# Kernel optimization log

Hardware: AMD Instinct MI355X
Metric: run time of the kernel (lower is better)

The kernel has to match this reference:

```python
import jax, jax.numpy as jnp
import numpy as np

N = 100000
E = 1600000
IN_C = 128
HID = 32
HEADS = 4
OUT_C = 16
G = 128
NEG_SLOPE = 0.2


def setup_inputs() -> dict:
    key = jax.random.key(0)
    ks = jax.random.split(key, 16)
    x = jax.random.normal(ks[0], (N, IN_C), dtype=jnp.float32)
    edge_index = jax.random.randint(ks[1], (2, E), 0, N, dtype=jnp.int64)
    batch = jnp.sort(jax.random.randint(ks[2], (N,), 0, G, dtype=jnp.int64))
    node_weights = jax.random.uniform(ks[3], (N, 1), dtype=jnp.float32)
    s = 1.0 / np.sqrt(IN_C)
    W1 = jax.random.uniform(ks[4], (IN_C, HEADS * HID), jnp.float32, -s, s)
    att_src1 = jax.random.uniform(ks[5], (HEADS, HID), jnp.float32, -s, s)
    att_dst1 = jax.random.uniform(ks[6], (HEADS, HID), jnp.float32, -s, s)
    b1 = jnp.zeros((HEADS * HID,), jnp.float32)
    s2 = 1.0 / np.sqrt(HEADS * HID)
    W2 = jax.random.uniform(ks[7], (HEADS * HID, HID), jnp.float32, -s2, s2)
    att_src2 = jax.random.uniform(ks[8], (1, HID), jnp.float32, -s2, s2)
    att_dst2 = jax.random.uniform(ks[9], (1, HID), jnp.float32, -s2, s2)
    b2 = jnp.zeros((HID,), jnp.float32)
    s3 = 1.0 / np.sqrt(HID)
    fcW = jax.random.uniform(ks[10], (HID, OUT_C), jnp.float32, -s3, s3)
    fcb = jax.random.uniform(ks[11], (OUT_C,), jnp.float32, -s3, s3)
    return {"x": x, "edge_index": edge_index, "batch": batch,
            "node_weights": node_weights,
            "W1": W1, "att_src1": att_src1, "att_dst1": att_dst1, "b1": b1,
            "W2": W2, "att_src2": att_src2, "att_dst2": att_dst2, "b2": b2,
            "fcW": fcW, "fcb": fcb}


def gat_conv(x, src, dst, W, att_src, att_dst, bias, heads, ch, concat):
    n = x.shape[0]
    h = (x @ W).reshape(n, heads, ch)                       # [N,H,C]
    a_src = jnp.sum(h * att_src[None], axis=-1)             # [N,H]
    a_dst = jnp.sum(h * att_dst[None], axis=-1)             # [N,H]
    e = jax.nn.leaky_relu(a_src[src] + a_dst[dst], NEG_SLOPE)  # [E,H]
    # segment softmax over incoming edges of each destination node
    e_max = jax.ops.segment_max(e, dst, num_segments=n)
    ex = jnp.exp(e - e_max[dst])
    denom = jax.ops.segment_sum(ex, dst, num_segments=n)
    alpha = ex / denom[dst]                                 # [E,H]
    msg = h[src] * alpha[..., None]                         # [E,H,C]
    out = jax.ops.segment_sum(msg, dst, num_segments=n)     # [N,H,C]
    if concat:
        out = out.reshape(n, heads * ch)
    else:
        out = out.mean(axis=1)
    return out + bias


def reference(x, edge_index, batch, node_weights,
              W1, att_src1, att_dst1, b1,
              W2, att_src2, att_dst2, b2,
              fcW, fcb):
    n = x.shape[0]
    # PyG GATConv adds self-loops by default
    loop = jnp.arange(n, dtype=edge_index.dtype)
    src = jnp.concatenate([edge_index[0], loop])
    dst = jnp.concatenate([edge_index[1], loop])

    h = x * node_weights
    h = jax.nn.elu(gat_conv(h, src, dst, W1, att_src1, att_dst1, b1, HEADS, HID, True))
    h = jax.nn.elu(gat_conv(h, src, dst, W2, att_src2, att_dst2, b2, 1, HID, False))
    # global mean pool over graphs
    sums = jax.ops.segment_sum(h, batch, num_segments=G)
    cnts = jax.ops.segment_sum(jnp.ones((n,), h.dtype), batch, num_segments=G)
    pooled = sums / jnp.maximum(cnts, 1.0)[:, None]
    return pooled @ fcW + fcb
```

## Files before the change

kernel.cpp:

```cpp
#include <hip/hip_runtime.h>
#include <cstdint>

#define NGRAPH 128
#define NEG 0.2f
#define NB_MAX 512
#define BSH 8
#define BSZ 256
#define CAP 8192
#define CH  2048

typedef unsigned int uint;
typedef unsigned short ushort;
typedef unsigned char uchar;
typedef __attribute__((ext_vector_type(8))) short bf16x8;
typedef __attribute__((ext_vector_type(4))) float f32x4;
typedef __attribute__((ext_vector_type(2))) float f32x2;

union U4B { uint4 u; bf16x8 v; };

__device__ __forceinline__ ushort f2bf(float f) {
  uint u = __float_as_uint(f);
  uint r = (u + 0x7FFF + ((u >> 16) & 1)) >> 16;
  return (ushort)r;
}

__device__ __forceinline__ uint cvtpkbf16(float lo, float hi) {
  uint r;
  asm("v_cvt_pk_bf16_f32 %0, %1, %2" : "=v"(r) : "v"(lo), "v"(hi));
  return r;
}

__device__ __forceinline__ void pkfma(f32x2& acc, f32x2 f, f32x2 w) {
  asm("v_pk_fma_f32 %0, %1, %2, %0" : "+v"(acc) : "v"(f), "v"(w));
}

__device__ __forceinline__ float bperm_f(int addr, float v) {
  return __int_as_float(__builtin_amdgcn_ds_bpermute(addr, __float_as_int(v)));
}
__device__ __forceinline__ int bperm_i(int addr, int v) {
  return __builtin_amdgcn_ds_bpermute(addr, v);
}

__device__ __forceinline__ int wave_incl_scan_i(int v) {
  int lane = threadIdx.x & 63;
#pragma unroll
  for (int off = 1; off < 64; off <<= 1) {
    int u = __shfl_up(v, off, 64);
    if (lane >= off) v += u;
  }
  return v;
}

__global__ void k_bin(const int* __restrict__ ei,
                      const float* __restrict__ W1, const float* __restrict__ W2,
                      ushort* __restrict__ Wt1, ushort* __restrict__ Wt2,
                      int E, int Etot, int NB, int nbin,
                      int* __restrict__ bcur, uint* __restrict__ bbuf) {
  if (blockIdx.x >= (uint)nbin) {
    int t2 = (blockIdx.x - nbin) * 256 + threadIdx.x;
    if (t2 < 16384) {
      int n = t2 >> 7, k = t2 & 127;
      Wt1[t2] = f2bf(W1[k * 128 + n]);
    } else {
      int u = t2 - 16384;
      int n = u >> 7, k = u & 127;
      Wt2[u] = f2bf(W2[k * 32 + n]);
    }
    return;
  }
  __shared__ int h[NB_MAX];
  __shared__ int baseo[NB_MAX];
  __shared__ uint crec[CH];
  __shared__ ushort cbkt[CH];
  int t = threadIdx.x;
  for (int b = t; b < NB; b += 256) h[b] = 0;
  __syncthreads();
  int cbase = blockIdx.x * CH;
  int cend = min(cbase + CH, Etot);
  int nch = cend - cbase;
  for (int i = t; i < nch; i += 256) {
    int e = cbase + i;
    int s, d;
    if (e < E) {
      s = __builtin_nontemporal_load(&ei[e]);
      d = __builtin_nontemporal_load(&ei[E + e]);
    } else { s = e - E; d = s; }
    int b = d >> BSH;
    crec[i] = ((uint)(d & (BSZ - 1)) << 17) | (uint)s;
    cbkt[i] = (ushort)b;
    atomicAdd(&h[b], 1);
  }
  __syncthreads();
  for (int b = t; b < NB; b += 256) {
    int c = h[b];
    baseo[b] = c ? atomicAdd(&bcur[b], c) : 0;
    h[b] = 0;
  }
  __syncthreads();
  for (int i = t; i < nch; i += 256) {
    int b = cbkt[i];
    int r = atomicAdd(&h[b], 1);
    bbuf[(size_t)b * CAP + baseo[b] + r] = crec[i];
  }
}

__global__ void k_bg(const uint* __restrict__ bbuf, const int* __restrict__ bcur,
                     int NB, int N, int* __restrict__ offs, int* __restrict__ ssrc,
                     const float* __restrict__ x, const ushort* __restrict__ Wt,
                     const float* __restrict__ nw, const float* __restrict__ att_s,
                     const float* __restrict__ att_d, uchar* __restrict__ hb1,
                     float* __restrict__ asrc, float* __restrict__ adst) {
  __shared__ int sst[NB_MAX + 1];
  __shared__ int wsum2[4];
  __shared__ int deg[BSZ];
  if (blockIdx.x < (uint)NB) {
    int t = threadIdx.x, lane = t & 63, wid = t >> 6;
    int v0 = (2 * t < NB) ? bcur[2 * t] : 0;
    int v1 = (2 * t + 1 < NB) ? bcur[2 * t + 1] : 0;
    int s = v0 + v1;
    int sv = wave_incl_scan_i(s);
    if (lane == 63) wsum2[wid] = sv;
    deg[t] = 0;
    __syncthreads();
    if (t == 0) {
      int r = 0;
#pragma unroll
      for (int k = 0; k < 4; k++) { int x2 = wsum2[k]; wsum2[k] = r; r += x2; }
    }
    __syncthreads();
    int excl = wsum2[wid] + sv - s;
    sst[2 * t] = excl;
    sst[2 * t + 1] = excl + v0;
    if (t == 255) sst[512] = excl + v0 + v1;
    __syncthreads();
    int b = blockIdx.x;
    int ebeg = sst[b], eend = sst[b + 1];
    int cnt = eend - ebeg;
    const uint* brow = bbuf + (size_t)b * CAP;
    for (int i = t; i < cnt; i += BSZ)
      atomicAdd(&deg[brow[i] >> 17], 1);
    __syncthreads();
    int v = deg[t];
    int sv2 = wave_incl_scan_i(v);
    if (lane == 63) wsum2[wid] = sv2;
    __syncthreads();
    if (t == 0) {
      int r = 0;
#pragma unroll
      for (int k = 0; k < 4; k++) { int x2 = wsum2[k]; wsum2[k] = r; r += x2; }
    }
    __syncthreads();
    int excl2 = wsum2[wid] + sv2 - v;
    int node = (b << BSH) + t;
    if (node < N) offs[node] = ebeg + excl2;
    if (b == 0 && t == 0) offs[N] = sst[512];
    __syncthreads();
    deg[t] = excl2;
    __syncthreads();
    for (int i = t; i < cnt; i += BSZ) {
      uint rec = brow[i];
      int r = atomicAdd(&deg[rec >> 17], 1);
      ssrc[ebeg + r] = (int)(rec & 0x1FFFF);
    }
    return;
  }
  int bid = blockIdx.x - NB;
  int wv = threadIdx.x >> 6, l = threadIdx.x & 63;
  int lg = l >> 4, lr = l & 15;
  int row0 = bid * 64 + wv * 16;
  int node = row0 + lr;
  bool valid = node < N;
  float sc = valid ? nw[node] : 0.f;
  bf16x8 xfr[4];
  const float* xr = x + (size_t)node * 128;
#pragma unroll
  for (int kc = 0; kc < 4; kc++) {
    float v[8];
    if (valid) {
      f32x4 q0 = __builtin_nontemporal_load(reinterpret_cast<const f32x4*>(xr + kc * 32 + lg * 8));
      f32x4 q1 = __builtin_nontemporal_load(reinterpret_cast<const f32x4*>(xr + kc * 32 + lg * 8 + 4));
      v[0] = q0[0]; v[1] = q0[1]; v[2] = q0[2]; v[3] = q0[3];
      v[4] = q1[0]; v[5] = q1[1]; v[6] = q1[2]; v[7] = q1[3];
    } else {
#pragma unroll
      for (int j = 0; j < 8; j++) v[j] = 0.f;
    }
    U4B a;
    a.u.x = cvtpkbf16(v[0] * sc, v[1] * sc);
    a.u.y = cvtpkbf16(v[2] * sc, v[3] * sc);
    a.u.z = cvtpkbf16(v[4] * sc, v[5] * sc);
    a.u.w = cvtpkbf16(v[6] * sc, v[7] * sc);
    xfr[kc] = a.v;
  }
  float pS[4] = {}, pD[4] = {};
#pragma unroll
  for (int ct = 0; ct < 8; ct++) {
    f32x4 acc = {0.f, 0.f, 0.f, 0.f};
    const ushort* wrow = Wt + (size_t)(ct * 16 + lr) * 128;
#pragma unroll
    for (int kc = 0; kc < 4; kc++) {
      U4B bfr;
      bfr.u = *reinterpret_cast<const uint4*>(wrow + kc * 32 + lg * 8);
      acc = __builtin_amdgcn_mfma_f32_16x16x32_bf16(bfr.v, xfr[kc], acc, 0, 0, 0);
    }
    int c0 = ct * 16 + lg * 4;
    if (valid) {
      uint u8 = (uint)__builtin_amdgcn_cvt_pk_fp8_f32(acc[0], acc[1], 0, false);
      u8 = (uint)__builtin_amdgcn_cvt_pk_fp8_f32(acc[2], acc[3], u8, true);
      *reinterpret_cast<uint*>(hb1 + (size_t)node * 128 + c0) = u8;
    }
    float4 as4 = *reinterpret_cast<const float4*>(att_s + c0);
    float4 ad4 = *reinterpret_cast<const float4*>(att_d + c0);
    int h = ct >> 1;
    pS[h] += acc[0] * as4.x + acc[1] * as4.y + acc[2] * as4.z + acc[3] * as4.w;
    pD[h] += acc[0] * ad4.x + acc[1] * ad4.y + acc[2] * ad4.z + acc[3] * ad4.w;
  }
#pragma unroll
  for (int off = 16; off < 64; off <<= 1) {
#pragma unroll
    for (int h = 0; h < 4; h++) {
      pS[h] += __shfl_xor(pS[h], off, 64);
      pD[h] += __shfl_xor(pD[h], off, 64);
    }
  }
  if (lg == 0 && valid) {
    *reinterpret_cast<float4*>(asrc + node * 4) = make_float4(pS[0], pS[1], pS[2], pS[3]);
    *reinterpret_cast<float4*>(adst + node * 4) = make_float4(pD[0], pD[1], pD[2], pD[3]);
  }
}

__global__ void k_aggr1(const int* __restrict__ offs, const int* __restrict__ ssrc,
                        const uchar* __restrict__ hb, const float* __restrict__ asrc,
                        const float* __restrict__ adst, const float* __restrict__ bias,
                        const ushort* __restrict__ Wt2, const float* __restrict__ as2,
                        const float* __restrict__ ad2, uchar* __restrict__ rec2,
                        float* __restrict__ adst2, int N) {
  __shared__ ushort rowl[4][136];
  int tid = threadIdx.x;
  int wv = tid >> 6, l = tid & 63;
  int d = blockIdx.x * 4 + wv;
  int dc = min(d, N - 1);
  int slot = l >> 3;
  int cb = l & 7;
  int h = cb >> 1;
  int hq = l & 3;
  int eidx = l >> 2;
  float adq = adst[dc * 4 + hq];
  int beg = offs[dc], end = offs[dc + 1];
  int endm1 = end - 1;
  const uchar* hbc = hb + cb * 16;
  int bp0 = (slot * 4 + h) << 2;
  int bp1 = bp0 + 128;
  f32x2 a2[8] = {};
  float dsp = 0.f;
  auto ACC = [&](uint4 p, float w) {
    f32x2 wp = {w, w};
    f32x2 f;
    f = __builtin_amdgcn_cvt_pk_f32_fp8(p.x, false); pkfma(a2[0], f, wp);
    f = __builtin_amdgcn_cvt_pk_f32_fp8(p.x, true);  pkfma(a2[1], f, wp);
    f = __builtin_amdgcn_cvt_pk_f32_fp8(p.y, false); pkfma(a2[2], f, wp);
    f = __builtin_amdgcn_cvt_pk_f32_fp8(p.y, true);  pkfma(a2[3], f, wp);
    f = __builtin_amdgcn_cvt_pk_f32_fp8(p.z, false); pkfma(a2[4], f, wp);
    f = __builtin_amdgcn_cvt_pk_f32_fp8(p.z, true);  pkfma(a2[5], f, wp);
    f = __builtin_amdgcn_cvt_pk_f32_fp8(p.w, false); pkfma(a2[6], f, wp);
    f = __builtin_amdgcn_cvt_pk_f32_fp8(p.w, true);  pkfma(a2[7], f, wp);
  };
  for (int base = beg; base < end; base += 32) {
    int eA = base + eidx;
    int eB = eA + 16;
    int sA = ssrc[min(eA, endm1)];
    int sB = ssrc[min(eB, endm1)];
    int s0 = bperm_i(bp0, sA);
    int s1 = bperm_i(bp1, sA);
    int s2 = bperm_i(bp0, sB);
    int s3 = bperm_i(bp1, sB);
    int rem = end - base;
    uint4 p0, p1, p2, p3;
    p0 = *reinterpret_cast<const uint4*>(hbc + (size_t)s0 * 128);
    if (rem > 8)  p1 = *reinterpret_cast<const uint4*>(hbc + (size_t)s1 * 128);
    if (rem > 16) p2 = *reinterpret_cast<const uint4*>(hbc + (size_t)s2 * 128);
    if (rem > 24) p3 = *reinterpret_cast<const uint4*>(hbc + (size_t)s3 * 128);
    float aA = asrc[sA * 4 + hq] + adq;
    float aB = asrc[sB * 4 + hq] + adq;
    aA = fmaxf(aA, aA * NEG);
    aB = fmaxf(aB, aB * NEG);
    float wA = (eA < end) ? __expf(aA) : 0.f;
    float wB = (eB < end) ? __expf(aB) : 0.f;
    dsp += wA + wB;
    float w0 = bperm_f(bp0, wA);
    float w1 = bperm_f(bp1, wA);
    float w2 = bperm_f(bp0, wB);
    float w3 = bperm_f(bp1, wB);
    ACC(p0, w0);
    if (rem > 8)  ACC(p1, w1);
    if (rem > 16) ACC(p2, w2);
    if (rem > 24) ACC(p3, w3);
  }
  dsp += __shfl_xor(dsp, 4, 64);
  dsp += __shfl_xor(dsp, 8, 64);
  dsp += __shfl_xor(dsp, 16, 64);
  dsp += __shfl_xor(dsp, 32, 64);
  float ds = bperm_f(h << 2, dsp);
  int b3 = (l >> 3) & 1, b4 = (l >> 4) & 1, b5 = (l >> 5) & 1;
  float t8[8];
#pragma unroll
  for (int r = 0; r < 8; r++) {
    float av = a2[r >> 1][r & 1];
    float bv = a2[(r + 8) >> 1][r & 1];
    float send = b3 ? av : bv;
    float recv = __shfl_xor(send, 8, 64);
    t8[r] = (b3 ? bv : av) + recv;
  }
  float t4[4];
#pragma unroll
  for (int r = 0; r < 4; r++) {
    float send = b4 ? t8[r] : t8[r + 4];
    float recv = __shfl_xor(send, 16, 64);
    t4[r] = (b4 ? t8[r + 4] : t8[r]) + recv;
  }
  float t2[2];
#pragma unroll
  for (int r = 0; r < 2; r++) {
    float send = b5 ? t4[r] : t4[r + 2];
    float recv = __shfl_xor(send, 32, 64);
    t2[r] = (b5 ? t4[r + 2] : t4[r]) + recv;
  }
  float inv = __builtin_amdgcn_rcpf(ds > 0.f ? ds : 1.f);
  int c0 = cb * 16 + b3 * 8 + b4 * 4 + b5 * 2;
  float2 bi = *reinterpret_cast<const float2*>(bias + c0);
  float r0 = fmaf(t2[0], inv, bi.x);
  float r1 = fmaf(t2[1], inv, bi.y);
  r0 = r0 > 0.f ? r0 : __expf(r0) - 1.f;
  r1 = r1 > 0.f ? r1 : __expf(r1) - 1.f;
  *reinterpret_cast<uint*>(&rowl[wv][c0]) = cvtpkbf16(r0, r1);
  __syncthreads();
  if (wv != 0) return;
  int lg = l >> 4, lr = l & 15;
  int rsel = lr & 3;
  bf16x8 bfrag[4];
#pragma unroll
  for (int kc = 0; kc < 4; kc++) {
    U4B bb;
    bb.u = *reinterpret_cast<const uint4*>(&rowl[rsel][kc * 32 + lg * 8]);
    bfrag[kc] = bb.v;
  }
  int dd = blockIdx.x * 4 + lr;
  bool vs = (lr < 4) && (dd < N);
  float pS = 0.f, pD = 0.f;
#pragma unroll
  for (int ct = 0; ct < 2; ct++) {
    f32x4 acc = {0.f, 0.f, 0.f, 0.f};
    const ushort* wrow = Wt2 + (size_t)(ct * 16 + lr) * 128;
#pragma unroll
    for (int kc = 0; kc < 4; kc++) {
      U4B bfr;
      bfr.u = *reinterpret_cast<const uint4*>(wrow + kc * 32 + lg * 8);
      acc = __builtin_amdgcn_mfma_f32_16x16x32_bf16(bfr.v, bfrag[kc], acc, 0, 0, 0);
    }
    int cg = ct * 16 + lg * 4;
    if (vs) {
      uint u8 = (uint)__builtin_amdgcn_cvt_pk_fp8_f32(acc[0], acc[1], 0, false);
      u8 = (uint)__builtin_amdgcn_cvt_pk_fp8_f32(acc[2], acc[3], u8, true);
      *reinterpret_cast<uint*>(rec2 + (size_t)dd * 64 + cg) = u8;
    }
    float4 as4 = *reinterpret_cast<const float4*>(as2 + cg);
    float4 ad4 = *reinterpret_cast<const float4*>(ad2 + cg);
    pS += acc[0] * as4.x + acc[1] * as4.y + acc[2] * as4.z + acc[3] * as4.w;
    pD += acc[0] * ad4.x + acc[1] * ad4.y + acc[2] * ad4.z + acc[3] * ad4.w;
  }
  pS += __shfl_xor(pS, 16, 64);
  pS += __shfl_xor(pS, 32, 64);
  pD += __shfl_xor(pD, 16, 64);
  pD += __shfl_xor(pD, 32, 64);
  if (vs && lg == 0) {
    *reinterpret_cast<float*>(rec2 + (size_t)dd * 64 + 32) = pS;
    adst2[dd] = pD;
  }
}

__global__ void k_aggr2(const int* __restrict__ offs, const int* __restrict__ ssrc,
                        const uchar* __restrict__ rec, const float* __restrict__ adst,
                        const float* __restrict__ bias, const int* __restrict__ batch,
                        float* __restrict__ gsum, int N) {
  __shared__ float sblk[4][32];
  int tid = threadIdx.x;
  int wid = tid >> 6, l = tid & 63;
  if (tid < 128) sblk[tid >> 5][tid & 31] = 0.f;
  __syncthreads();
  int d = blockIdx.x * 4 + wid;
  bool valid = d < N;
  int dc = valid ? d : N - 1;
  int slot = l >> 2;
  int k = l & 3;
  float ad = adst[dc];
  int beg = offs[dc];
  int end = valid ? offs[dc + 1] : beg;
  int endm1 = end - 1;
  const uchar* rk = rec + k * 8;
  int bq0 = slot << 2;
  int bq1 = (slot + 16) << 2;
  int bq2 = (slot + 32) << 2;
  int bq3 = (slot + 48) << 2;
  f32x2 a2[4] = {};
  float dsp = 0.f;
  auto ACC2 = [&](uint2 p, float w) {
    f32x2 wp = {w, w};
    f32x2 f;
    f = __builtin_amdgcn_cvt_pk_f32_fp8(p.x, false); pkfma(a2[0], f, wp);
    f = __builtin_amdgcn_cvt_pk_f32_fp8(p.x, true);  pkfma(a2[1], f, wp);
    f = __builtin_amdgcn_cvt_pk_f32_fp8(p.y, false); pkfma(a2[2], f, wp);
    f = __builtin_amdgcn_cvt_pk_f32_fp8(p.y, true);  pkfma(a2[3], f, wp);
  };
  for (int base = beg; base < end; base += 64) {
    int e = base + l;
    int sL = ssrc[min(e, endm1)];
    int s0 = bperm_i(bq0, sL);
    int s1 = bperm_i(bq1, sL);
    int s2 = bperm_i(bq2, sL);
    int s3 = bperm_i(bq3, sL);
    int rem = end - base;
    float av = *reinterpret_cast<const float*>(rec + (size_t)sL * 64 + 32);
    uint2 p0, p1, p2, p3;
    p0 = *reinterpret_cast<const uint2*>(rk + (size_t)s0 * 64);
    if (rem > 16) p1 = *reinterpret_cast<const uint2*>(rk + (size_t)s1 * 64);
    if (rem > 32) p2 = *reinterpret_cast<const uint2*>(rk + (size_t)s2 * 64);
    if (rem > 48) p3 = *reinterpret_cast<const uint2*>(rk + (size_t)s3 * 64);
    float xv = av + ad;
    xv = fmaxf(xv, xv * NEG);
    float wL = (e < end) ? __expf(xv) : 0.f;
    dsp += wL;
    float w0 = bperm_f(bq0, wL);
    float w1 = bperm_f(bq1, wL);
    float w2 = bperm_f(bq2, wL);
    float w3 = bperm_f(bq3, wL);
    ACC2(p0, w0);
    if (rem > 16) ACC2(p1, w1);
    if (rem > 32) ACC2(p2, w2);
    if (rem > 48) ACC2(p3, w3);
  }
  dsp += __shfl_xor(dsp, 1, 64);
  dsp += __shfl_xor(dsp, 2, 64);
  dsp += __shfl_xor(dsp, 4, 64);
  dsp += __shfl_xor(dsp, 8, 64);
  dsp += __shfl_xor(dsp, 16, 64);
  dsp += __shfl_xor(dsp, 32, 64);
  int b2 = (l >> 2) & 1, b3 = (l >> 3) & 1, b4 = (l >> 4) & 1;
  float t4[4];
#pragma unroll
  for (int r = 0; r < 4; r++) {
    float av = a2[r >> 1][r & 1];
    float bv = a2[(r + 4) >> 1][r & 1];
    float send = b2 ? av : bv;
    float recv = __shfl_xor(send, 4, 64);
    t4[r] = (b2 ? bv : av) + recv;
  }
  float t2[2];
#pragma unroll
  for (int r = 0; r < 2; r++) {
    float send = b3 ? t4[r] : t4[r + 2];
    float recv = __shfl_xor(send, 8, 64);
    t2[r] = (b3 ? t4[r + 2] : t4[r]) + recv;
  }
  float send = b4 ? t2[0] : t2[1];
  float recv = __shfl_xor(send, 16, 64);
  float t1 = (b4 ? t2[1] : t2[0]) + recv;
  t1 += __shfl_xor(t1, 32, 64);
  int gfirst = batch[blockIdx.x * 4];
  if (l < 32 && valid) {
    int c = k * 8 + b2 * 4 + b3 * 2 + b4;
    float inv = __builtin_amdgcn_rcpf(dsp > 0.f ? dsp : 1.f);
    float r = fmaf(t1, inv, bias[c]);
    r = r > 0.f ? r : __expf(r) - 1.f;
    int g = batch[dc];
    int sl = g - gfirst;
    if (sl < 4) atomicAdd(&sblk[sl][c], r);
    else atomicAdd(&gsum[g * 32 + c], r);
  }
  __syncthreads();
  if (tid < 128) {
    int sl = tid >> 5, c = tid & 31;
    float v = sblk[sl][c];
    int gg = gfirst + sl;
    if (v != 0.f && gg < NGRAPH) atomicAdd(&gsum[gg * 32 + c], v);
  }
}

__global__ void k_fc(const float* __restrict__ gsum, const int* __restrict__ batch,
                     const float* __restrict__ fcW, const float* __restrict__ fcb,
                     float* __restrict__ out, int N) {
  int g = blockIdx.x;
  int l = threadIdx.x;
  int lo = 0, hi = N;
  while (lo < hi) { int mid = (lo + hi) >> 1; if (batch[mid] < g) lo = mid + 1; else hi = mid; }
  int beg = lo;
  hi = N;
  while (lo < hi) { int mid = (lo + hi) >> 1; if (batch[mid] < g + 1) lo = mid + 1; else hi = mid; }
  int end = lo;
  float inv = 1.f / fmaxf((float)(end - beg), 1.f);
  __shared__ float pooled[32];
  if (l < 32) pooled[l] = gsum[g * 32 + l] * inv;
  __syncthreads();
  if (l < 16) {
    float r = fcb[l];
#pragma unroll
    for (int cc = 0; cc < 32; cc++) r += pooled[cc] * fcW[cc * 16 + l];
    out[g * 16 + l] = r;
  }
}

extern "C" void kernel_launch(void* const* d_in, const int* in_sizes, int n_in,
                              void* d_out, int out_size, void* d_ws, size_t ws_size,
                              hipStream_t stream) {
  const float* x     = (const float*)d_in[0];
  const int*   ei    = (const int*)d_in[1];
  const int*   batch = (const int*)d_in[2];
  const float* nw    = (const float*)d_in[3];
  const float* W1    = (const float*)d_in[4];
  const float* as1w  = (const float*)d_in[5];
  const float* ad1w  = (const float*)d_in[6];
  const float* b1    = (const float*)d_in[7];
  const float* W2    = (const float*)d_in[8];
  const float* as2w  = (const float*)d_in[9];
  const float* ad2w  = (const float*)d_in[10];
  const float* b2    = (const float*)d_in[11];
  const float* fcW   = (const float*)d_in[12];
  const float* fcb   = (const float*)d_in[13];
  float* out = (float*)d_out;

  const int N = in_sizes[0] / 128;
  const int E = in_sizes[1] / 2;
  const int Etot = E + N;
  const int NB = (N + BSZ - 1) >> BSH;

  char* w = (char*)d_ws;
  size_t ofs = 0;
  auto alloc = [&](size_t bytes) {
    char* p = w + ofs;
    ofs += (bytes + 255) & ~(size_t)255;
    return p;
  };
  uchar*  hb1    = (uchar*)alloc((size_t)N * 128);
  uchar*  rec2   = (uchar*)alloc((size_t)N * 64);
  float*  asrc1  = (float*)alloc((size_t)N * 4 * 4);
  float*  adst1  = (float*)alloc((size_t)N * 4 * 4);
  float*  adst2  = (float*)alloc((size_t)N * 4);
  ushort* Wt1    = (ushort*)alloc(16384 * 2);
  ushort* Wt2    = (ushort*)alloc(4096 * 2);
  int*    bcur   = (int*)alloc((size_t)NB * 4);
  float*  gsum   = (float*)alloc((size_t)NGRAPH * 32 * 4);
  int*    offs   = (int*)alloc((size_t)(N + 1) * 4);
  uint*   bbuf   = (uint*)alloc((size_t)NB * CAP * 4);
  int*    ssrc   = (int*)alloc((size_t)Etot * 4);

  size_t zlen = (size_t)((char*)gsum - (char*)bcur) + (size_t)NGRAPH * 32 * 4;
  hipMemsetAsync(bcur, 0, zlen, stream);

  const int nbin = (Etot + CH - 1) / CH;
  k_bin<<<nbin + 80, 256, 0, stream>>>(ei, W1, W2, Wt1, Wt2, E, Etot, NB, nbin, bcur, bbuf);

  const int ngemm1 = (N + 63) / 64;
  k_bg<<<NB + ngemm1, 256, 0, stream>>>(bbuf, bcur, NB, N, offs, ssrc,
                                        x, Wt1, nw, as1w, ad1w, hb1, asrc1, adst1);

  k_aggr1<<<(N + 3) / 4, 256, 0, stream>>>(offs, ssrc, hb1, asrc1, adst1, b1,
                                           Wt2, as2w, ad2w, rec2, adst2, N);

  k_aggr2<<<(N + 3) / 4, 256, 0, stream>>>(offs, ssrc, rec2, adst2, b2, batch, gsum, N);

  k_fc<<<NGRAPH, 64, 0, stream>>>(gsum, batch, fcW, fcb, out, N);
}
```

Before: 305.7 us.

## Widen CSR buckets to 512 nodes and cache bucket records in LDS

Doubles the destination bucket size to 512 nodes, which halves the number of buckets, and doubles the per-bin chunk size in the binning kernel. The CSR build kernel now handles two nodes per thread in its scan. It also caches up to 6144 bucket records in shared memory during the degree pass, so the scatter pass reads them from there instead of global memory a second time. This means fewer, larger blocks and higher LDS use (about 24KB more), which may lower occupancy and parallelism in the build stage.

```diff
diff --git a/kernel.cpp b/kernel.cpp
--- a/kernel.cpp
+++ b/kernel.cpp
@@ -4,10 +4,11 @@
 #define NGRAPH 128
 #define NEG 0.2f
 #define NB_MAX 512
-#define BSH 8
-#define BSZ 256
-#define CAP 8192
-#define CH  2048
+#define BSH 9
+#define BSZ 512
+#define CAP 16384
+#define RC  6144
+#define CH  4096
 
 typedef unsigned int uint;
 typedef unsigned short ushort;
@@ -71,7 +72,7 @@
   __shared__ int h[NB_MAX];
   __shared__ int baseo[NB_MAX];
   __shared__ uint crec[CH];
-  __shared__ ushort cbkt[CH];
+  __shared__ uchar cbkt[CH];
   int t = threadIdx.x;
   for (int b = t; b < NB; b += 256) h[b] = 0;
   __syncthreads();
@@ -87,7 +88,7 @@
     } else { s = e - E; d = s; }
     int b = d >> BSH;
     crec[i] = ((uint)(d & (BSZ - 1)) << 17) | (uint)s;
-    cbkt[i] = (ushort)b;
+    cbkt[i] = (uchar)b;
     atomicAdd(&h[b], 1);
   }
   __syncthreads();
@@ -113,6 +114,7 @@
   __shared__ int sst[NB_MAX + 1];
   __shared__ int wsum2[4];
   __shared__ int deg[BSZ];
+  __shared__ uint rcache[RC];
   if (blockIdx.x < (uint)NB) {
     int t = threadIdx.x, lane = t & 63, wid = t >> 6;
     int v0 = (2 * t < NB) ? bcur[2 * t] : 0;
@@ -121,6 +123,7 @@
     int sv = wave_incl_scan_i(s);
     if (lane == 63) wsum2[wid] = sv;
     deg[t] = 0;
+    deg[t + 256] = 0;
     __syncthreads();
     if (t == 0) {
       int r = 0;
@@ -137,11 +140,15 @@
     int ebeg = sst[b], eend = sst[b + 1];
     int cnt = eend - ebeg;
     const uint* brow = bbuf + (size_t)b * CAP;
-    for (int i = t; i < cnt; i += BSZ)
-      atomicAdd(&deg[brow[i] >> 17], 1);
-    __syncthreads();
-    int v = deg[t];
-    int sv2 = wave_incl_scan_i(v);
+    for (int i = t; i < cnt; i += 256) {
+      uint rec = brow[i];
+      if (i < RC) rcache[i] = rec;
+      atomicAdd(&deg[rec >> 17], 1);
+    }
+    __syncthreads();
+    int u0 = deg[2 * t], u1 = deg[2 * t + 1];
+    int s2 = u0 + u1;
+    int sv2 = wave_incl_scan_i(s2);
     if (lane == 63) wsum2[wid] = sv2;
     __syncthreads();
     if (t == 0) {
@@ -150,15 +157,17 @@
       for (int k = 0; k < 4; k++) { int x2 = wsum2[k]; wsum2[k] = r; r += x2; }
     }
     __syncthreads();
-    int excl2 = wsum2[wid] + sv2 - v;
-    int node = (b << BSH) + t;
-    if (node < N) offs[node] = ebeg + excl2;
+    int excl2 = wsum2[wid] + sv2 - s2;
+    int node0 = (b << BSH) + 2 * t;
+    if (node0 < N)     offs[node0]     = ebeg + excl2;
+    if (node0 + 1 < N) offs[node0 + 1] = ebeg + excl2 + u0;
     if (b == 0 && t == 0) offs[N] = sst[512];
     __syncthreads();
-    deg[t] = excl2;
-    __syncthreads();
-    for (int i = t; i < cnt; i += BSZ) {
-      uint rec = brow[i];
+    deg[2 * t]     = excl2;
+    deg[2 * t + 1] = excl2 + u0;
+    __syncthreads();
+    for (int i = t; i < cnt; i += 256) {
+      uint rec = (i < RC) ? rcache[i] : brow[i];
       int r = atomicAdd(&deg[rec >> 17], 1);
       ssrc[ebeg + r] = (int)(rec & 0x1FFFF);
     }
```

Measured after the change: 299.5 us. 1.02x faster.
